# Optimization experiments

Measured on AMD Instinct MI355X. Metric: run time of the kernel, lower is better.

## Reference

```python
import jax, jax.numpy as jnp
import numpy as np

D_IN, D_K, D_V, N_HEADS = 1024, 64, 64, 16
B, S = 4, 2048


def setup_inputs() -> dict:
    key = jax.random.key(0)
    ks = jax.random.split(key, 9)
    scale = 1.0 / np.sqrt(D_IN)
    return {
        "X": jax.random.normal(ks[0], (B, S, D_IN), dtype=jnp.float32),
        # per-head projection weights, stacked over heads: [H, d_in, d]
        "Wq": jax.random.normal(ks[1], (N_HEADS, D_IN, D_K), dtype=jnp.float32) * scale,
        "bq": jax.random.normal(ks[2], (N_HEADS, D_K), dtype=jnp.float32) * 0.02,
        "Wk": jax.random.normal(ks[3], (N_HEADS, D_IN, D_K), dtype=jnp.float32) * scale,
        "bk": jax.random.normal(ks[4], (N_HEADS, D_K), dtype=jnp.float32) * 0.02,
        "Wv": jax.random.normal(ks[5], (N_HEADS, D_IN, D_V), dtype=jnp.float32) * scale,
        "bv": jax.random.normal(ks[6], (N_HEADS, D_V), dtype=jnp.float32) * 0.02,
        # output projection: [H*d_v, d_in]
        "Wo": jax.random.normal(ks[7], (N_HEADS * D_V, D_IN), dtype=jnp.float32) * (1.0 / np.sqrt(N_HEADS * D_V)),
        "bo": jax.random.normal(ks[8], (D_IN,), dtype=jnp.float32) * 0.02,
    }


def reference(X, Wq, bq, Wk, bk, Wv, bv, Wo, bo):
    # Per-head linear projections, all heads batched: [B,H,S,d]
    Q = jnp.einsum('bsd,hdk->bhsk', X, Wq) + bq[None, :, None, :]
    K = jnp.einsum('bsd,hdk->bhsk', X, Wk) + bk[None, :, None, :]
    V = jnp.einsum('bsd,hdv->bhsv', X, Wv) + bv[None, :, None, :]

    d_k = Q.shape[-1]
    scores = jnp.einsum('bhsk,bhtk->bhst', Q, K) / jnp.sqrt(jnp.float32(d_k))

    S_len = X.shape[1]
    causal = jnp.tril(jnp.ones((S_len, S_len), dtype=bool))  # [S,S]
    scores = jnp.where(causal[None, None, :, :], scores, -jnp.inf)
    P = jax.nn.softmax(scores, axis=-1)

    A = jnp.einsum('bhst,bhtv->bhsv', P, V)        # [B,H,S,d_v]
    # concat heads along feature dim (head-major order matches torch cat over heads)
    A = A.transpose(0, 2, 1, 3).reshape(X.shape[0], S_len, -1)  # [B,S,H*d_v]
    return A @ Wo + bo
```

## Files before the change

### kernel.cpp

```cpp
#include <hip/hip_runtime.h>
#include <cstdint>
#include <cstddef>

typedef __attribute__((ext_vector_type(4))) float f32x4;
typedef __attribute__((ext_vector_type(8))) short s16x8;
typedef __attribute__((ext_vector_type(4))) short s16x4;
typedef __attribute__((ext_vector_type(4))) int i32x4;

#define DEV __device__ __forceinline__

DEV short f2bf(float f) {
    unsigned u = __builtin_bit_cast(unsigned, f);
    unsigned r = (u + 0x7FFFu + ((u >> 16) & 1u)) >> 16;
    return (short)r;
}

DEV float bf2f(short s) {
    return __builtin_bit_cast(float, ((unsigned)(unsigned short)s) << 16);
}

DEV void gload_lds16(const void* g, void* l) {
    __builtin_amdgcn_global_load_lds(
        (const __attribute__((address_space(1))) unsigned int*)g,
        (__attribute__((address_space(3))) unsigned int*)l, 16, 0, 0);
}


__global__ void k_cvt_x(const float* __restrict__ X, short* __restrict__ Xb, int n4) {
    int stride = gridDim.x * blockDim.x;
    for (int i = blockIdx.x * blockDim.x + threadIdx.x; i < n4; i += stride) {
        f32x4 v = *(const f32x4*)&X[i * 4];
        s16x4 s;
#pragma unroll
        for (int j = 0; j < 4; ++j) s[j] = f2bf(v[j]);
        *(s16x4*)&Xb[i * 4] = s;
    }
}

__global__ void k_pack_wqkv_t(const float* __restrict__ Wq, const float* __restrict__ Wk,
                              const float* __restrict__ Wv, short* __restrict__ Wbt) {
    __shared__ float tileT[64][65];
    const int bx = blockIdx.x, tid = threadIdx.x;
    const int t = bx >> 8, h = (bx >> 4) & 15, dc = bx & 15;
    const float* W = (t == 0) ? Wq : (t == 1) ? Wk : Wv;
    const float* src = W + ((size_t)h * 1024 + dc * 64) * 64;
#pragma unroll
    for (int i = 0; i < 4; ++i) {
        int idx4 = i * 256 + tid;
        f32x4 v = *(const f32x4*)&src[idx4 * 4];
        int flat = idx4 * 4;
        int d = flat >> 6, k0 = flat & 63;
#pragma unroll
        for (int q = 0; q < 4; ++q) tileT[k0 + q][d] = v[q];
    }
    __syncthreads();
    const int k = tid >> 2, d4 = (tid & 3) * 16;
    s16x8 o0, o1;
#pragma unroll
    for (int q = 0; q < 8; ++q) {
        o0[q] = f2bf(tileT[k][d4 + q]);
        o1[q] = f2bf(tileT[k][d4 + 8 + q]);
    }
    size_t c = (size_t)t * 1024 + h * 64 + k;
    *(s16x8*)&Wbt[c * 1024 + dc * 64 + d4] = o0;
    *(s16x8*)&Wbt[c * 1024 + dc * 64 + d4 + 8] = o1;
}

__global__ void k_pack_wo_t(const float* __restrict__ Wo, short* __restrict__ Wobt) {
    __shared__ float tileT[64][65];
    const int bx = blockIdx.x, tid = threadIdx.x;
    const int c0 = (bx >> 4) * 64, n0 = (bx & 15) * 64;
    const int r = tid >> 2, cch = tid & 3;
#pragma unroll
    for (int it = 0; it < 4; ++it) {
        int colf = cch * 4 + it * 16;
        f32x4 v = *(const f32x4*)&Wo[(size_t)(c0 + r) * 1024 + n0 + colf];
#pragma unroll
        for (int q = 0; q < 4; ++q) tileT[colf + q][r] = v[q];
    }
    __syncthreads();
    const int n = tid >> 2, c4 = (tid & 3) * 16;
    s16x8 o0, o1;
#pragma unroll
    for (int q = 0; q < 8; ++q) {
        o0[q] = f2bf(tileT[n][c4 + q]);
        o1[q] = f2bf(tileT[n][c4 + 8 + q]);
    }
    *(s16x8*)&Wobt[(size_t)(n0 + n) * 1024 + c0 + c4] = o0;
    *(s16x8*)&Wobt[(size_t)(n0 + n) * 1024 + c0 + c4 + 8] = o1;
}


template <int EPI>
__launch_bounds__(256)
__global__ void gemm_bf16(const short* __restrict__ Ag, const short* __restrict__ Btg,
                          const float* __restrict__ b0, const float* __restrict__ b1,
                          const float* __restrict__ b2,
                          short* __restrict__ O0, short* __restrict__ O1, short* __restrict__ O2,
                          float* __restrict__ Of) {
    __shared__ short As[128 * 64];
    __shared__ short Bs[128 * 64];
    const int tid = threadIdx.x;
    const int wave = tid >> 6, lane = tid & 63;
    const int wm = wave >> 1, wn = wave & 1;
    const int m0 = blockIdx.y * 128, n0 = blockIdx.x * 128;

    f32x4 acc[4][4] = {};

    const int lr = lane >> 3;
    const int cb = (lane & 7) * 16;
    const int cl = cb ^ (lr << 4);

    for (int kt = 0; kt < 16; ++kt) {
        __syncthreads();
#pragma unroll
        for (int i = 0; i < 4; ++i) {
            int r8 = wave * 32 + i * 8;
            const char* ga = (const char*)(Ag + (size_t)(m0 + r8 + lr) * 1024 + kt * 64) + cl;
            gload_lds16(ga, &As[r8 * 64]);
            const char* gb = (const char*)(Btg + (size_t)(n0 + r8 + lr) * 1024 + kt * 64) + cl;
            gload_lds16(gb, &Bs[r8 * 64]);
        }
        asm volatile("s_waitcnt vmcnt(0)" ::: "memory");
        __syncthreads();
#pragma unroll
        for (int ks = 0; ks < 2; ++ks) {
            int kb = ks * 64 + (lane >> 4) * 16;
            s16x8 af[4], bf[4];
#pragma unroll
            for (int mf = 0; mf < 4; ++mf) {
                int m = wm * 64 + mf * 16 + (lane & 15);
                af[mf] = *(const s16x8*)&As[m * 64 + ((kb ^ ((m & 7) << 4)) >> 1)];
            }
#pragma unroll
            for (int nf = 0; nf < 4; ++nf) {
                int n = wn * 64 + nf * 16 + (lane & 15);
                bf[nf] = *(const s16x8*)&Bs[n * 64 + ((kb ^ ((n & 7) << 4)) >> 1)];
            }
#pragma unroll
            for (int mf = 0; mf < 4; ++mf)
#pragma unroll
                for (int nf = 0; nf < 4; ++nf)
                    acc[mf][nf] = __builtin_amdgcn_mfma_f32_16x16x32_bf16(af[mf], bf[nf],
                                                                          acc[mf][nf], 0, 0, 0);
        }
    }

    if (EPI == 0) {
#pragma unroll
        for (int nf = 0; nf < 4; ++nf) {
            int n = n0 + wn * 64 + nf * 16 + (lane & 15);
            int t = n >> 10;
            int h = (n >> 6) & 15;
            int kk = n & 63;
            const float* bias = (t == 0) ? b0 : (t == 1) ? b1 : b2;
            short* dst = (t == 0) ? O0 : (t == 1) ? O1 : O2;
            float scale = (t == 0) ? 0.1803368851f : 1.0f;
            float bb = bias[h * 64 + kk];
#pragma unroll
            for (int mf = 0; mf < 4; ++mf) {
#pragma unroll
                for (int r = 0; r < 4; ++r) {
                    int m = m0 + wm * 64 + mf * 16 + (lane >> 4) * 4 + r;
                    int b_ = m >> 11, sp = m & 2047;
                    float v = (acc[mf][nf][r] + bb) * scale;
                    dst[(((size_t)(b_ * 16 + h)) * 2048 + sp) * 64 + kk] = f2bf(v);
                }
            }
        }
    } else {
#pragma unroll
        for (int nf = 0; nf < 4; ++nf) {
            int n = n0 + wn * 64 + nf * 16 + (lane & 15);
            float bb = b0[n];
#pragma unroll
            for (int mf = 0; mf < 4; ++mf) {
#pragma unroll
                for (int r = 0; r < 4; ++r) {
                    int m = m0 + wm * 64 + mf * 16 + (lane >> 4) * 4 + r;
                    Of[(size_t)m * 1024 + n] = acc[mf][nf][r] + bb;
                }
            }
        }
    }
}


#define STAGE_K(KT, OFF) do {                                                   \
    _Pragma("unroll")                                                           \
    for (int i_ = 0; i_ < 2; ++i_) {                                            \
        int l_ = wave * 16 + i_ * 8 + lr;          \
        int gr_ = (((l_ >> 4) & 1) << 5) | (((l_ >> 2) & 3) << 3) |             \
                  (((l_ >> 5) & 1) << 2) | (l_ & 3);        \
        const char* g_ = (const char*)(Kb + base + (size_t)((KT) * 64 + gr_) * 64) + cl; \
        gload_lds16(g_, &KsAll[(OFF) + (wave * 16 + i_ * 8) * 64]);             \
    } } while (0)

#define LOAD_V(KT) do {                                                         \
    const short* vs_ = Vb + base + (size_t)((KT) * 64 + 2 * kp) * 64 + vb8 * 8; \
    v0_ = *(const s16x8*)vs_;                                                   \
    v1_ = *(const s16x8*)(vs_ + 64); } while (0)

#define WRITE_V(OFF) do {                                                       \
    _Pragma("unroll")                                                           \
    for (int j_ = 0; j_ < 8; ++j_) {                                            \
        int v_ = vb8 * 8 + j_;                                                  \
        unsigned pk_ = (unsigned)(unsigned short)v0_[j_] |                      \
                       ((unsigned)(unsigned short)v1_[j_] << 16);               \
        int bo_ = (4 * kp) ^ ((v_ & 7) << 4);                                   \
        *(unsigned*)((char*)&VtAll[(OFF) + v_ * 64] + bo_) = pk_;               \
    } } while (0)

#define STRIP2_COMPUTE(KT, OFF) do {                                            \
    f32x4 scL_[4], scS_[4];                                                     \
    _Pragma("unroll")                                                           \
    for (int nf_ = 0; nf_ < 4; ++nf_)                                           \
        _Pragma("unroll")                                                       \
        for (int r_ = 0; r_ < 4; ++r_) { scL_[nf_][r_] = -10.f; scS_[nf_][r_] = -10.f; } \
    __builtin_amdgcn_s_setprio(1);                                              \
    _Pragma("unroll")                                                           \
    for (int ks_ = 0; ks_ < 2; ++ks_) {                                         \
        int kb_ = ks_ * 64 + (lane >> 4) * 16;                                  \
        _Pragma("unroll")                                                       \
        for (int nf_ = 0; nf_ < 4; ++nf_) {                                     \
            int key_ = nf_ * 16 + (lane & 15);                                  \
            s16x8 bf_ = *(const s16x8*)&KsAll[(OFF) + key_ * 64 + ((kb_ ^ ((key_ & 7) << 4)) >> 1)]; \
            scL_[nf_] = __builtin_amdgcn_mfma_f32_16x16x32_bf16(bf_, qL_[ks_], scL_[nf_], 0, 0, 0); \
            scS_[nf_] = __builtin_amdgcn_mfma_f32_16x16x32_bf16(bf_, qS_[ks_], scS_[nf_], 0, 0, 0); \
        }                                                                       \
    }                                                                           \
    __builtin_amdgcn_s_setprio(0);                                              \
    if ((KT) == QTSv_) {                                   \
        int qq_ = wave * 16 + (lane & 15);                                      \
        int g8_ = (lane >> 4) * 8;                                              \
        _Pragma("unroll")                                                       \
        for (int nf_ = 0; nf_ < 4; ++nf_) {                                     \
            _Pragma("unroll")                                                   \
            for (int r_ = 0; r_ < 4; ++r_) {                                    \
                int key_ = ((nf_ & 1) << 5) + g8_ + ((nf_ >> 1) << 2) + r_;     \
                if (key_ > qq_) scS_[nf_][r_] = NEG_INF;                        \
            }                                                                   \
        }                                                                       \
    }                                                                           \
    _Pragma("unroll")                                                           \
    for (int nf_ = 0; nf_ < 4; ++nf_)                                           \
        _Pragma("unroll")                                                       \
        for (int r_ = 0; r_ < 4; ++r_) {                                        \
            scL_[nf_][r_] = exp2f(scL_[nf_][r_]);                               \
            scS_[nf_][r_] = exp2f(scS_[nf_][r_]);                               \
        }                                                                       \
    unsigned pdL_[4][2], pdS_[4][2];                                            \
    _Pragma("unroll")                                                           \
    for (int nf_ = 0; nf_ < 4; ++nf_) {                                         \
        asm("v_cvt_pk_bf16_f32 %0, %1, %2"                                      \
            : "=v"(pdL_[nf_][0]) : "v"(scL_[nf_][0]), "v"(scL_[nf_][1]));       \
        asm("v_cvt_pk_bf16_f32 %0, %1, %2"                                      \
            : "=v"(pdL_[nf_][1]) : "v"(scL_[nf_][2]), "v"(scL_[nf_][3]));       \
        asm("v_cvt_pk_bf16_f32 %0, %1, %2"                                      \
            : "=v"(pdS_[nf_][0]) : "v"(scS_[nf_][0]), "v"(scS_[nf_][1]));       \
        asm("v_cvt_pk_bf16_f32 %0, %1, %2"                                      \
            : "=v"(pdS_[nf_][1]) : "v"(scS_[nf_][2]), "v"(scS_[nf_][3]));       \
    }                                                                           \
    __builtin_amdgcn_s_setprio(1);                                              \
    _Pragma("unroll")                                                           \
    for (int ks_ = 0; ks_ < 2; ++ks_) {                                         \
        i32x4 piL_, piS_;                                                       \
        piL_[0] = (int)pdL_[ks_][0]; piL_[1] = (int)pdL_[ks_][1];               \
        piL_[2] = (int)pdL_[ks_ + 2][0]; piL_[3] = (int)pdL_[ks_ + 2][1];       \
        piS_[0] = (int)pdS_[ks_][0]; piS_[1] = (int)pdS_[ks_][1];               \
        piS_[2] = (int)pdS_[ks_ + 2][0]; piS_[3] = (int)pdS_[ks_ + 2][1];       \
        s16x8 paL_ = __builtin_bit_cast(s16x8, piL_);                           \
        s16x8 paS_ = __builtin_bit_cast(s16x8, piS_);                           \
        lsumL_ = __builtin_amdgcn_mfma_f32_16x16x32_bf16(paL_, onesf, lsumL_, 0, 0, 0); \
        lsumS_ = __builtin_amdgcn_mfma_f32_16x16x32_bf16(paS_, onesf, lsumS_, 0, 0, 0); \
        int kb_ = ks_ * 64 + (lane >> 4) * 16;                                  \
        _Pragma("unroll")                                                       \
        for (int nf_ = 0; nf_ < 4; ++nf_) {                                     \
            int v_ = nf_ * 16 + (lane & 15);                                    \
            s16x8 vf_ = *(const s16x8*)&VtAll[(OFF) + v_ * 64 + ((kb_ ^ ((v_ & 7) << 4)) >> 1)]; \
            oL_[nf_] = __builtin_amdgcn_mfma_f32_16x16x32_bf16(paL_, vf_, oL_[nf_], 0, 0, 0); \
            oS_[nf_] = __builtin_amdgcn_mfma_f32_16x16x32_bf16(paS_, vf_, oS_[nf_], 0, 0, 0); \
        }                                                                       \
    }                                                                           \
    __builtin_amdgcn_s_setprio(0);                                              \
    } while (0)

#define STRIP_COMPUTE(QF, O, LSUM, OFF) do {                                    \
    f32x4 sc_[4];                                                               \
    _Pragma("unroll")                                                           \
    for (int nf_ = 0; nf_ < 4; ++nf_)                                           \
        _Pragma("unroll")                                                       \
        for (int r_ = 0; r_ < 4; ++r_) sc_[nf_][r_] = -10.f;                    \
    __builtin_amdgcn_s_setprio(1);                                              \
    _Pragma("unroll")                                                           \
    for (int ks_ = 0; ks_ < 2; ++ks_) {                                         \
        int kb_ = ks_ * 64 + (lane >> 4) * 16;                                  \
        _Pragma("unroll")                                                       \
        for (int nf_ = 0; nf_ < 4; ++nf_) {                                     \
            int key_ = nf_ * 16 + (lane & 15);                                  \
            s16x8 bf_ = *(const s16x8*)&KsAll[(OFF) + key_ * 64 + ((kb_ ^ ((key_ & 7) << 4)) >> 1)]; \
            sc_[nf_] = __builtin_amdgcn_mfma_f32_16x16x32_bf16(bf_, QF[ks_], sc_[nf_], 0, 0, 0); \
        }                                                                       \
    }                                                                           \
    __builtin_amdgcn_s_setprio(0);                                              \
    {                                                                           \
        int qq_ = wave * 16 + (lane & 15);                                      \
        int g8_ = (lane >> 4) * 8;                                              \
        _Pragma("unroll")                                                       \
        for (int nf_ = 0; nf_ < 4; ++nf_) {                                     \
            _Pragma("unroll")                                                   \
            for (int r_ = 0; r_ < 4; ++r_) {                                    \
                int key_ = ((nf_ & 1) << 5) + g8_ + ((nf_ >> 1) << 2) + r_;     \
                if (key_ > qq_) sc_[nf_][r_] = NEG_INF;                         \
            }                                                                   \
        }                                                                       \
    }                                                                           \
    _Pragma("unroll")                                                           \
    for (int nf_ = 0; nf_ < 4; ++nf_)                                           \
        _Pragma("unroll")                                                       \
        for (int r_ = 0; r_ < 4; ++r_) sc_[nf_][r_] = exp2f(sc_[nf_][r_]);      \
    unsigned pd_[4][2];                                                         \
    _Pragma("unroll")                                                           \
    for (int nf_ = 0; nf_ < 4; ++nf_) {                                         \
        asm("v_cvt_pk_bf16_f32 %0, %1, %2"                                      \
            : "=v"(pd_[nf_][0]) : "v"(sc_[nf_][0]), "v"(sc_[nf_][1]));          \
        asm("v_cvt_pk_bf16_f32 %0, %1, %2"                                      \
            : "=v"(pd_[nf_][1]) : "v"(sc_[nf_][2]), "v"(sc_[nf_][3]));          \
    }                                                                           \
    __builtin_amdgcn_s_setprio(1);                                              \
    _Pragma("unroll")                                                           \
    for (int ks_ = 0; ks_ < 2; ++ks_) {                                         \
        i32x4 pi_;                                                              \
        pi_[0] = (int)pd_[ks_][0]; pi_[1] = (int)pd_[ks_][1];                   \
        pi_[2] = (int)pd_[ks_ + 2][0]; pi_[3] = (int)pd_[ks_ + 2][1];           \
        s16x8 pa_ = __builtin_bit_cast(s16x8, pi_);                             \
        LSUM = __builtin_amdgcn_mfma_f32_16x16x32_bf16(pa_, onesf, LSUM, 0, 0, 0); \
        int kb_ = ks_ * 64 + (lane >> 4) * 16;                                  \
        _Pragma("unroll")                                                       \
        for (int nf_ = 0; nf_ < 4; ++nf_) {                                     \
            int v_ = nf_ * 16 + (lane & 15);                                    \
            s16x8 vf_ = *(const s16x8*)&VtAll[(OFF) + v_ * 64 + ((kb_ ^ ((v_ & 7) << 4)) >> 1)]; \
            O[nf_] = __builtin_amdgcn_mfma_f32_16x16x32_bf16(pa_, vf_, O[nf_], 0, 0, 0); \
        }                                                                       \
    }                                                                           \
    __builtin_amdgcn_s_setprio(0);                                              \
    } while (0)

#define ITERB(T) do {                                                           \
    const bool st_ = ((T) + 1 < hi_);                                           \
    if (st_) { STAGE_K((T) + 1, off1_); LOAD_V((T) + 1); }                      \
    STRIP2_COMPUTE((T), off0_);                                                 \
    asm volatile("s_waitcnt vmcnt(0)" ::: "memory");                            \
    if (st_) WRITE_V(off1_);                                                    \
    asm volatile("s_waitcnt lgkmcnt(0)" ::: "memory");                          \
    __builtin_amdgcn_s_barrier();                                               \
    int tmp_ = off0_; off0_ = off1_; off1_ = tmp_;                              \
} while (0)

#define PEPILOGUE(SOFF, O, LSUM) do {                                           \
    _Pragma("unroll")                                                           \
    for (int r_ = 0; r_ < 4; ++r_) {                                            \
        int row_ = (SOFF) + wave * 16 + (lane >> 4) * 4 + r_;                   \
        if ((lane & 15) == 0) Lp_[row_] = LSUM[r_];                             \
        _Pragma("unroll")                                                       \
        for (int nf_ = 0; nf_ < 4; ++nf_)                                       \
            Op_[row_ * 64 + nf_ * 16 + (lane & 15)] = f2bf(O[nf_][r_]);         \
    } } while (0)

__launch_bounds__(256)
__global__ void attn_fwd(const short* __restrict__ Qb, const short* __restrict__ Kb,
                         const short* __restrict__ Vb, short* __restrict__ Opart,
                         float* __restrict__ Lpart) {
    __shared__ short KsAll[2 * 64 * 64];
    __shared__ short VtAll[2 * 64 * 64];
    const int tid = threadIdx.x, wave = tid >> 6, lane = tid & 63;
    const int hx = blockIdx.x;
    const int y = blockIdx.y;
    const int jj = 15 - (y >> 1);
    const int half = y & 1;
    const int lo_ = half * (jj + 1);
    const int hi_ = lo_ + jj + 1;
    const int QTSv_ = 2 * jj, QTLv_ = 2 * jj + 1;
    const int ND_ = ((hi_ < QTLv_) ? hi_ : QTLv_) - lo_;
    const bool tail_ = (hi_ > QTLv_);
    const size_t base = (size_t)hx * 2048 * 64;
    const float NEG_INF = -__builtin_inff();

    const int qrow = wave * 16 + (lane & 15);
    const int qoff = (lane >> 4) * 8;
    const int lr = lane >> 3, cl = ((lane & 7) * 16) ^ (lr << 4);
    const int kp = tid & 31;
    const int vb8 = tid >> 5;

    const s16x8 onesf = {(short)0x3F80, (short)0x3F80, (short)0x3F80, (short)0x3F80,
                         (short)0x3F80, (short)0x3F80, (short)0x3F80, (short)0x3F80};

    s16x8 qL_[2], qS_[2];
#pragma unroll
    for (int ks = 0; ks < 2; ++ks) {
        qL_[ks] = *(const s16x8*)&Qb[base + (size_t)(QTLv_ * 64 + qrow) * 64 + ks * 32 + qoff];
        qS_[ks] = *(const s16x8*)&Qb[base + (size_t)(QTSv_ * 64 + qrow) * 64 + ks * 32 + qoff];
    }

    f32x4 oL_[4] = {}, oS_[4] = {};
    f32x4 lsumL_ = {}, lsumS_ = {};
    s16x8 v0_, v1_;
    int off0_ = 0, off1_ = 4096;

    STAGE_K(lo_, off0_);
    LOAD_V(lo_);
    asm volatile("s_waitcnt vmcnt(0)" ::: "memory");
    WRITE_V(off0_);
    asm volatile("s_waitcnt lgkmcnt(0)" ::: "memory");
    __builtin_amdgcn_s_barrier();

    for (int t_ = lo_; t_ < lo_ + ND_; ++t_) {
        ITERB(t_);
    }
    if (tail_) {
        STRIP_COMPUTE(qL_, oL_, lsumL_, off0_);
    }

    const int slot_ = (hx * 16 + jj) * 2 + half;
    short* Op_ = Opart + (size_t)slot_ * 8192;
    float* Lp_ = Lpart + (size_t)slot_ * 128;
    PEPILOGUE(0, oS_, lsumS_);
    PEPILOGUE(64, oL_, lsumL_);
}

__launch_bounds__(256)
__global__ void attn_combine(const short* __restrict__ Opart, const float* __restrict__ Lpart,
                             short* __restrict__ Ab) {
    const int bx = blockIdx.x, t = threadIdx.x;
    const int hx = bx >> 4, jj = bx & 15;
    const int b_ = hx >> 4, h = hx & 15;
    const short* O0 = Opart + (size_t)((hx * 16 + jj) * 2) * 8192;
    const short* O1 = O0 + 8192;
    const float* L0 = Lpart + (size_t)((hx * 16 + jj) * 2) * 128;
    const float* L1 = L0 + 128;
    const int c4 = (t & 15) * 4;
#pragma unroll
    for (int p = 0; p < 8; ++p) {
        int row = (t >> 4) + p * 16;
        float rl = 1.0f / (L0[row] + L1[row]);
        s16x4 a = *(const s16x4*)&O0[row * 64 + c4];
        s16x4 b = *(const s16x4*)&O1[row * 64 + c4];
        s16x4 o;
#pragma unroll
        for (int q = 0; q < 4; ++q) o[q] = f2bf((bf2f(a[q]) + bf2f(b[q])) * rl);
        int qglob = jj * 128 + row;
        *(s16x4*)&Ab[((size_t)(b_ * 2048 + qglob)) * 1024 + h * 64 + c4] = o;
    }
}


extern "C" void kernel_launch(void* const* d_in, const int* in_sizes, int n_in,
                              void* d_out, int out_size, void* d_ws, size_t ws_size,
                              hipStream_t stream) {
    const float* X  = (const float*)d_in[0];
    const float* Wq = (const float*)d_in[1];
    const float* bq = (const float*)d_in[2];
    const float* Wk = (const float*)d_in[3];
    const float* bk = (const float*)d_in[4];
    const float* Wv = (const float*)d_in[5];
    const float* bv = (const float*)d_in[6];
    const float* Wo = (const float*)d_in[7];
    const float* bo = (const float*)d_in[8];
    float* out = (float*)d_out;
    char* ws = (char*)d_ws;

    short* Wobt  = (short*)(ws);
    short* Qb    = (short*)(ws + 2097152);
    short* Kb    = (short*)(ws + 18874368);
    short* Vb    = (short*)(ws + 35651584);
    short* Ab    = (short*)(ws + 52428800);
    short* Xb    = (short*)(ws + 69206016);
    short* Wbt   = (short*)(ws + 85983232);
    short* Opart = (short*)(ws + 69206016);
    float* Lpart = (float*)(ws + 102760448);

    k_cvt_x<<<2048, 256, 0, stream>>>(X, Xb, 8192 * 1024 / 4);
    k_pack_wqkv_t<<<768, 256, 0, stream>>>(Wq, Wk, Wv, Wbt);
    k_pack_wo_t<<<256, 256, 0, stream>>>(Wo, Wobt);

    gemm_bf16<0><<<dim3(24, 64), 256, 0, stream>>>(Xb, Wbt, bq, bk, bv, Qb, Kb, Vb, nullptr);
    attn_fwd<<<dim3(64, 32), 256, 0, stream>>>(Qb, Kb, Vb, Opart, Lpart);
    attn_combine<<<1024, 256, 0, stream>>>(Opart, Lpart, Ab);
    gemm_bf16<1><<<dim3(8, 64), 256, 0, stream>>>(Ab, Wobt, bo, nullptr, nullptr,
                                                  nullptr, nullptr, nullptr, out);
}
```

Measured before the change: 189.7 us.

## Load K fragments directly into registers instead of staging through LDS

```diff
diff --git a/kernel.cpp b/kernel.cpp
--- a/kernel.cpp
+++ b/kernel.cpp
@@ -186,15 +186,15 @@
 }
 
 
-#define STAGE_K(KT, OFF) do {                                                   \
-    _Pragma("unroll")                                                           \
-    for (int i_ = 0; i_ < 2; ++i_) {                                            \
-        int l_ = wave * 16 + i_ * 8 + lr;          \
-        int gr_ = (((l_ >> 4) & 1) << 5) | (((l_ >> 2) & 3) << 3) |             \
-                  (((l_ >> 5) & 1) << 2) | (l_ & 3);        \
-        const char* g_ = (const char*)(Kb + base + (size_t)((KT) * 64 + gr_) * 64) + cl; \
-        gload_lds16(g_, &KsAll[(OFF) + (wave * 16 + i_ * 8) * 64]);             \
-    } } while (0)
+#define LOAD_K(KT) do {                                                         \
+    const short* kt_ = Kb + base + (size_t)(KT) * 4096;                         \
+    _Pragma("unroll")                                                           \
+    for (int ks_ = 0; ks_ < 2; ++ks_)                                           \
+        _Pragma("unroll")                                                       \
+        for (int nf_ = 0; nf_ < 4; ++nf_)                                       \
+            kf_[ks_][nf_] = *(const s16x8*)&kt_[kvb_ + (nf_ & 1) * 2048 +       \
+                                                (nf_ >> 1) * 256 + ks_ * 32];   \
+    } while (0)
 
 #define LOAD_V(KT) do {                                                         \
     const short* vs_ = Vb + base + (size_t)((KT) * 64 + 2 * kp) * 64 + vb8 * 8; \
@@ -211,25 +211,20 @@
         *(unsigned*)((char*)&VtAll[(OFF) + v_ * 64] + bo_) = pk_;               \
     } } while (0)
 
-#define STRIP2_COMPUTE(KT, OFF) do {                                            \
-    f32x4 scL_[4], scS_[4];                                                     \
-    _Pragma("unroll")                                                           \
-    for (int nf_ = 0; nf_ < 4; ++nf_)                                           \
-        _Pragma("unroll")                                                       \
-        for (int r_ = 0; r_ < 4; ++r_) { scL_[nf_][r_] = -10.f; scS_[nf_][r_] = -10.f; } \
+#define RAWEXP(X) asm("v_exp_f32 %0, %1" : "=v"(X) : "v"(X))
+
+#define STRIP2_COMPUTE(KT, OFF, ...) do {                                       \
+    f32x4 scL_[4] = {}, scS_[4] = {};                                           \
     __builtin_amdgcn_s_setprio(1);                                              \
     _Pragma("unroll")                                                           \
-    for (int ks_ = 0; ks_ < 2; ++ks_) {                                         \
-        int kb_ = ks_ * 64 + (lane >> 4) * 16;                                  \
+    for (int ks_ = 0; ks_ < 2; ++ks_)                                           \
         _Pragma("unroll")                                                       \
         for (int nf_ = 0; nf_ < 4; ++nf_) {                                     \
-            int key_ = nf_ * 16 + (lane & 15);                                  \
-            s16x8 bf_ = *(const s16x8*)&KsAll[(OFF) + key_ * 64 + ((kb_ ^ ((key_ & 7) << 4)) >> 1)]; \
-            scL_[nf_] = __builtin_amdgcn_mfma_f32_16x16x32_bf16(bf_, qL_[ks_], scL_[nf_], 0, 0, 0); \
-            scS_[nf_] = __builtin_amdgcn_mfma_f32_16x16x32_bf16(bf_, qS_[ks_], scS_[nf_], 0, 0, 0); \
-        }                                                                       \
-    }                                                                           \
+            scL_[nf_] = __builtin_amdgcn_mfma_f32_16x16x32_bf16(kf_[ks_][nf_], qL_[ks_], scL_[nf_], 0, 0, 0); \
+            scS_[nf_] = __builtin_amdgcn_mfma_f32_16x16x32_bf16(kf_[ks_][nf_], qS_[ks_], scS_[nf_], 0, 0, 0); \
+        }                                                                       \
     __builtin_amdgcn_s_setprio(0);                                              \
+    __VA_ARGS__;                                                                \
     if ((KT) == QTSv_) {                                   \
         int qq_ = wave * 16 + (lane & 15);                                      \
         int g8_ = (lane >> 4) * 8;                                              \
@@ -246,8 +241,8 @@
     for (int nf_ = 0; nf_ < 4; ++nf_)                                           \
         _Pragma("unroll")                                                       \
         for (int r_ = 0; r_ < 4; ++r_) {                                        \
-            scL_[nf_][r_] = exp2f(scL_[nf_][r_]);                               \
-            scS_[nf_][r_] = exp2f(scS_[nf_][r_]);                               \
+            RAWEXP(scL_[nf_][r_]);                                              \
+            RAWEXP(scS_[nf_][r_]);                                              \
         }                                                                       \
     unsigned pdL_[4][2], pdS_[4][2];                                            \
     _Pragma("unroll")                                                           \
@@ -286,22 +281,13 @@
     } while (0)
 
 #define STRIP_COMPUTE(QF, O, LSUM, OFF) do {                                    \
-    f32x4 sc_[4];                                                               \
-    _Pragma("unroll")                                                           \
-    for (int nf_ = 0; nf_ < 4; ++nf_)                                           \
-        _Pragma("unroll")                                                       \
-        for (int r_ = 0; r_ < 4; ++r_) sc_[nf_][r_] = -10.f;                    \
+    f32x4 sc_[4] = {};                                                          \
     __builtin_amdgcn_s_setprio(1);                                              \
     _Pragma("unroll")                                                           \
-    for (int ks_ = 0; ks_ < 2; ++ks_) {                                         \
-        int kb_ = ks_ * 64 + (lane >> 4) * 16;                                  \
-        _Pragma("unroll")                                                       \
-        for (int nf_ = 0; nf_ < 4; ++nf_) {                                     \
-            int key_ = nf_ * 16 + (lane & 15);                                  \
-            s16x8 bf_ = *(const s16x8*)&KsAll[(OFF) + key_ * 64 + ((kb_ ^ ((key_ & 7) << 4)) >> 1)]; \
-            sc_[nf_] = __builtin_amdgcn_mfma_f32_16x16x32_bf16(bf_, QF[ks_], sc_[nf_], 0, 0, 0); \
-        }                                                                       \
-    }                                                                           \
+    for (int ks_ = 0; ks_ < 2; ++ks_)                                           \
+        _Pragma("unroll")                                                       \
+        for (int nf_ = 0; nf_ < 4; ++nf_)                                       \
+            sc_[nf_] = __builtin_amdgcn_mfma_f32_16x16x32_bf16(kf_[ks_][nf_], QF[ks_], sc_[nf_], 0, 0, 0); \
     __builtin_amdgcn_s_setprio(0);                                              \
     {                                                                           \
         int qq_ = wave * 16 + (lane & 15);                                      \
@@ -318,7 +304,7 @@
     _Pragma("unroll")                                                           \
     for (int nf_ = 0; nf_ < 4; ++nf_)                                           \
         _Pragma("unroll")                                                       \
-        for (int r_ = 0; r_ < 4; ++r_) sc_[nf_][r_] = exp2f(sc_[nf_][r_]);      \
+        for (int r_ = 0; r_ < 4; ++r_) RAWEXP(sc_[nf_][r_]);                    \
     unsigned pd_[4][2];                                                         \
     _Pragma("unroll")                                                           \
     for (int nf_ = 0; nf_ < 4; ++nf_) {                                         \
@@ -348,9 +334,12 @@
 
 #define ITERB(T) do {                                                           \
     const bool st_ = ((T) + 1 < hi_);                                           \
-    if (st_) { STAGE_K((T) + 1, off1_); LOAD_V((T) + 1); }                      \
-    STRIP2_COMPUTE((T), off0_);                                                 \
-    asm volatile("s_waitcnt vmcnt(0)" ::: "memory");                            \
+    if (st_) LOAD_V((T) + 1);                                                   \
+    if (st_) {                                                                  \
+        STRIP2_COMPUTE((T), off0_, LOAD_K((T) + 1));                            \
+    } else {                                                                    \
+        STRIP2_COMPUTE((T), off0_, );                                           \
+    }                                                                           \
     if (st_) WRITE_V(off1_);                                                    \
     asm volatile("s_waitcnt lgkmcnt(0)" ::: "memory");                          \
     __builtin_amdgcn_s_barrier();                                               \
@@ -371,7 +360,6 @@
 __global__ void attn_fwd(const short* __restrict__ Qb, const short* __restrict__ Kb,
                          const short* __restrict__ Vb, short* __restrict__ Opart,
                          float* __restrict__ Lpart) {
-    __shared__ short KsAll[2 * 64 * 64];
     __shared__ short VtAll[2 * 64 * 64];
     const int tid = threadIdx.x, wave = tid >> 6, lane = tid & 63;
     const int hx = blockIdx.x;
@@ -388,9 +376,10 @@
 
     const int qrow = wave * 16 + (lane & 15);
     const int qoff = (lane >> 4) * 8;
-    const int lr = lane >> 3, cl = ((lane & 7) * 16) ^ (lr << 4);
     const int kp = tid & 31;
     const int vb8 = tid >> 5;
+
+    const int kvb_ = ((((lane & 15) >> 2) * 8 + (lane & 3)) * 64) + (lane >> 4) * 8;
 
     const s16x8 onesf = {(short)0x3F80, (short)0x3F80, (short)0x3F80, (short)0x3F80,
                          (short)0x3F80, (short)0x3F80, (short)0x3F80, (short)0x3F80};
@@ -404,12 +393,12 @@
 
     f32x4 oL_[4] = {}, oS_[4] = {};
     f32x4 lsumL_ = {}, lsumS_ = {};
+    s16x8 kf_[2][4];
     s16x8 v0_, v1_;
     int off0_ = 0, off1_ = 4096;
 
-    STAGE_K(lo_, off0_);
     LOAD_V(lo_);
-    asm volatile("s_waitcnt vmcnt(0)" ::: "memory");
+    LOAD_K(lo_);
     WRITE_V(off0_);
     asm volatile("s_waitcnt lgkmcnt(0)" ::: "memory");
     __builtin_amdgcn_s_barrier();
```

New measurement: 205.8 us. 1.08x slower.
